# Optimization experiments

Measured on AMD Instinct MI355X. Metric: run time of the kernel, lower is better.

The kernel has to match this reference:

```python
import jax, jax.numpy as jnp
import numpy as np

N_NODES = 50000
N_EDGES = 600000
IN_CH = 128
HID = 256
OUT_FEAT = 256
OUT_CH = 128
EPS = 1e-12


def _sage_conv(x, src, dst, mask_f, Wl, bl, Wr, n_nodes):
    # PyG SAGEConv: out = lin_l(mean_{j in N(i)} x_j) + lin_r(x_i); L2-normalize rows.
    msg = x[src] * mask_f[:, None]                                  # [E, d] gather
    agg = jax.ops.segment_sum(msg, dst, num_segments=n_nodes)      # [N, d]
    cnt = jax.ops.segment_sum(mask_f, dst, num_segments=n_nodes)   # [N]
    agg = agg / jnp.maximum(cnt, 1.0)[:, None]                      # mean over kept edges
    out = agg @ Wl.T + bl + x @ Wr.T                                 # [N, h]
    nrm = jnp.maximum(jnp.linalg.norm(out, axis=-1, keepdims=True), EPS)
    return out / nrm


def setup_inputs() -> dict:
    key = jax.random.key(0)
    ks = jax.random.split(key, 12)
    x = jax.random.normal(ks[0], (N_NODES, IN_CH), dtype=jnp.float32)
    edge_index = jax.random.randint(ks[1], (2, N_EDGES), 0, N_NODES, dtype=jnp.int32)
    edge_mask = jax.random.bernoulli(ks[2], 0.7, (N_EDGES,))  # dropout_edge p=0.3 keep mask

    def lin(k, fan_out, fan_in):
        s = 1.0 / np.sqrt(fan_in)
        return jax.random.uniform(k, (fan_out, fan_in), jnp.float32, -s, s)

    W1l = lin(ks[3], HID, IN_CH)
    b1 = jnp.zeros((HID,), jnp.float32)
    W1r = lin(ks[4], HID, IN_CH)
    Ws = lin(ks[5], HID, IN_CH)
    bs = jnp.zeros((HID,), jnp.float32)
    W2l = lin(ks[6], OUT_FEAT, HID)
    b2 = jnp.zeros((OUT_FEAT,), jnp.float32)
    W2r = lin(ks[7], OUT_FEAT, HID)
    Wo = lin(ks[8], OUT_CH, OUT_FEAT)
    bo = jnp.zeros((OUT_CH,), jnp.float32)
    return {"x": x, "edge_index": edge_index, "edge_mask": edge_mask,
            "W1l": W1l, "b1": b1, "W1r": W1r, "Ws": Ws, "bs": bs,
            "W2l": W2l, "b2": b2, "W2r": W2r, "Wo": Wo, "bo": bo}


def reference(x, edge_index, edge_mask, W1l, b1, W1r, Ws, bs, W2l, b2, W2r, Wo, bo):
    src, dst = edge_index[0], edge_index[1]
    ones = jnp.ones((src.shape[0],), x.dtype)
    # conv1 uses all edges
    h = _sage_conv(x, src, dst, ones, W1l, b1, W1r, N_NODES)
    h = h + (x @ Ws.T + bs)
    h = jnp.tanh(h)
    # conv2 uses edge-dropped graph (mask = kept edges)
    mask_f = edge_mask.astype(x.dtype)
    h = jnp.tanh(_sage_conv(h, src, dst, mask_f, W2l, b2, W2r, N_NODES))
    return h @ Wo.T + bo
```

## Files before the change

### kernel.cpp

```cpp
#include <hip/hip_runtime.h>
#include <hip/hip_bf16.h>

#define N_NODES 50000
#define N_PAD   50048
#define N_EDGES 600000
#define IN_CH 128
#define HID 256
#define OUT_CH 128

typedef unsigned short u16;
typedef unsigned char u8;
typedef unsigned int u32;

typedef __attribute__((ext_vector_type(8))) short short8;
typedef __attribute__((ext_vector_type(4))) float f32x4;

typedef __attribute__((address_space(3))) u32 as3_u32;
typedef __attribute__((address_space(1))) const u32 as1_u32;

__device__ __forceinline__ float bf2f(u16 v) {
    unsigned u = ((unsigned)v) << 16;
    return __uint_as_float(u);
}
__device__ __forceinline__ u16 f2bf(float f) {
    unsigned u = __float_as_uint(f);
    u += 0x7FFF + ((u >> 16) & 1);
    return (u16)(u >> 16);
}

__device__ __forceinline__ float fast_tanh(float x) {
    float e = __builtin_amdgcn_exp2f(x * 2.88539008177793f);
    return 1.f - 2.f * __builtin_amdgcn_rcpf(e + 1.f);
}

__device__ __forceinline__ void async16(const void* g, void* l) {
    __builtin_amdgcn_global_load_lds((as1_u32*)g, (as3_u32*)l, 16, 0, 0);
}

__global__ void detect_kernel(const u16* __restrict__ xu, const u8* __restrict__ mb,
                              int* __restrict__ flags) {
    int lane = threadIdx.x & 63;

    int inr = 0;
    {
        u32 w0 = ((const u32*)xu)[lane * 2 + 0];
        u32 w1 = ((const u32*)xu)[lane * 2 + 1];
        u16 h[4] = {(u16)w0, (u16)(w0 >> 16), (u16)w1, (u16)(w1 >> 16)};
#pragma unroll
        for (int j = 0; j < 4; j++) {
            int e = (h[j] >> 7) & 0xFF;
            if (e >= 100 && e <= 133) inr++;
        }
    }

    int c1 = 0, c23 = 0, h3f_1 = 0, h3f_3 = 0;
#pragma unroll
    for (int t = 0; t < 16; t++) {
        u32 w = ((const u32*)mb)[t * 64 + lane];
        u8 b1 = (u8)(w >> 8), b2 = (u8)(w >> 16), b3 = (u8)(w >> 24);
        if (b1) c1++;
        if (b1 == 0x3F) h3f_1 = 1;
        if (b2) c23++;
        if (b3) c23++;
        if (b3 == 0x3F) h3f_3 = 1;
    }

#pragma unroll
    for (int off = 32; off > 0; off >>= 1) {
        inr   += __shfl_xor(inr, off, 64);
        c1    += __shfl_xor(c1, off, 64);
        c23   += __shfl_xor(c23, off, 64);
        h3f_1 |= __shfl_xor(h3f_1, off, 64);
        h3f_3 |= __shfl_xor(h3f_3, off, 64);
    }

    if (lane == 0 && blockIdx.x == 0) {
        flags[0] = (inr >= 200) ? 1 : 0;
        int fmt;
        if (h3f_1) fmt = 3;
        else if (h3f_3) fmt = 2;
        else if (c1 + c23 > 0) fmt = 0;
        else fmt = 1;
        flags[1] = fmt;
    }
}

#define NX (N_NODES * IN_CH)
#define DEGP_N 50176
__global__ void convert_all_kernel(const void* __restrict__ x,
                                   const void* __restrict__ W1l, const void* __restrict__ W1r,
                                   const void* __restrict__ Ws,
                                   const void* __restrict__ W2l, const void* __restrict__ W2r,
                                   const void* __restrict__ Wo,
                                   const void* __restrict__ b1, const void* __restrict__ bs,
                                   const void* __restrict__ b2, const void* __restrict__ bo,
                                   u16* __restrict__ xb, u16* __restrict__ Wc1,
                                   u16* __restrict__ Wsb, u16* __restrict__ Wc2,
                                   u16* __restrict__ Wob, float* __restrict__ biasf,
                                   u32* __restrict__ degp,
                                   const int* __restrict__ flags) {
    int i = blockIdx.x * blockDim.x + threadIdx.x;
    int isbf = flags[0];
    auto cv = [&](const void* s, int idx) -> u16 {
        return isbf ? ((const u16*)s)[idx] : f2bf(((const float*)s)[idx]);
    };
    if (i < NX) { xb[i] = cv(x, i); return; }
    i -= NX;
    if (i < 256 * 256) {
        int n = i >> 8, k = i & 255;
        const void* s = (k < 128) ? W1l : W1r;
        Wc1[i] = cv(s, n * 128 + (k & 127));
        return;
    }
    i -= 256 * 256;
    if (i < 256 * 128) { Wsb[i] = cv(Ws, i); return; }
    i -= 256 * 128;
    if (i < 256 * 512) {
        int n = i >> 9, k = i & 511;
        const void* s = (k < 256) ? W2l : W2r;
        Wc2[i] = cv(s, n * 256 + (k & 255));
        return;
    }
    i -= 256 * 512;
    if (i < 128 * 256) { Wob[i] = cv(Wo, i); return; }
    i -= 128 * 256;
    if (i < 896) {
        const void* s; int idx;
        if (i < 256)      { s = b1; idx = i; }
        else if (i < 512) { s = bs; idx = i - 256; }
        else if (i < 768) { s = b2; idx = i - 512; }
        else              { s = bo; idx = i - 768; }
        biasf[i] = isbf ? bf2f(((const u16*)s)[idx]) : ((const float*)s)[idx];
        return;
    }
    i -= 896;
    if (i < DEGP_N) degp[i] = 0;
}
#define CONV_TOTAL (NX + 256 * 256 + 256 * 128 + 256 * 512 + 128 * 256 + 896 + DEGP_N)

__global__ void hist_kernel(const int* __restrict__ ei, const void* __restrict__ em,
                            u32* __restrict__ degp, u32* __restrict__ rankp,
                            const int* __restrict__ flags) {
    int i = blockIdx.x * blockDim.x + threadIdx.x;
    if (i >= N_EDGES) return;
    int d = ei[N_EDGES + i];
    int fmt = flags[1];
    bool keep;
    if (fmt == 0)      keep = ((const u8*)em)[i] != 0;
    else if (fmt == 1) keep = ((const int*)em)[i] != 0;
    else if (fmt == 2) keep = ((const float*)em)[i] != 0.f;
    else               keep = ((const u16*)em)[i] != 0;
    u32 inc = keep ? 0x10001u : 1u;
    u32 old = atomicAdd(&degp[d], inc);
    rankp[i] = (old & 0xffffu) | (keep ? (old & 0xffff0000u) : 0xffff0000u);
}

__global__ void partial_kernel(const u32* __restrict__ degp, u32* __restrict__ partial) {
    __shared__ u32 sh[256];
    int t = threadIdx.x;
    int i = blockIdx.x * 256 + t;
    sh[t] = (i < N_NODES) ? degp[i] : 0;
    __syncthreads();
    for (int s = 128; s > 0; s >>= 1) {
        if (t < s) sh[t] += sh[t + s];
        __syncthreads();
    }
    if (t == 0) partial[blockIdx.x] = sh[0];
}

__global__ void scanp_kernel(const u32* __restrict__ partial, int* __restrict__ pscan, int nb) {
    __shared__ int sh[256];
    int t = threadIdx.x;
    u32 pv = (t < nb) ? partial[t] : 0;
    int v1 = pv & 0xffff, v2 = pv >> 16;
    sh[t] = v1;
    __syncthreads();
    for (int o = 1; o < 256; o <<= 1) {
        int u = (t >= o) ? sh[t - o] : 0;
        __syncthreads();
        sh[t] += u;
        __syncthreads();
    }
    if (t < nb) pscan[t] = sh[t] - v1;
    __syncthreads();
    sh[t] = v2;
    __syncthreads();
    for (int o = 1; o < 256; o <<= 1) {
        int u = (t >= o) ? sh[t - o] : 0;
        __syncthreads();
        sh[t] += u;
        __syncthreads();
    }
    if (t < nb) pscan[nb + t] = sh[t] - v2;
}

__global__ void rowptr_kernel(const u32* __restrict__ degp, const int* __restrict__ pscan,
                              int* __restrict__ row_ptr, int* __restrict__ row_ptr2, int nb) {
    __shared__ u32 sh[256];
    int t = threadIdx.x;
    int i = blockIdx.x * 256 + t;
    u32 v = (i < N_NODES) ? degp[i] : 0;
    sh[t] = v;
    __syncthreads();
    for (int o = 1; o < 256; o <<= 1) {
        u32 u = (t >= o) ? sh[t - o] : 0;
        __syncthreads();
        sh[t] += u;
        __syncthreads();
    }
    u32 ex = sh[t] - v;
    if (i <= N_NODES) {
        row_ptr[i]  = pscan[blockIdx.x] + (int)(ex & 0xffff);
        row_ptr2[i] = pscan[nb + blockIdx.x] + (int)(ex >> 16);
    }
}

__global__ void scatter_csr_kernel(const int* __restrict__ ei, const u32* __restrict__ rankp,
                                   const int* __restrict__ row_ptr, const int* __restrict__ row_ptr2,
                                   int* __restrict__ srcs, int* __restrict__ srcs2) {
    int i = blockIdx.x * blockDim.x + threadIdx.x;
    if (i >= N_EDGES) return;
    int d = ei[N_EDGES + i];
    int s = ei[i];
    u32 rp = rankp[i];
    srcs[row_ptr[d] + (int)(rp & 0xffffu)] = s;
    u32 kr = rp >> 16;
    if (kr != 0xffffu) srcs2[row_ptr2[d] + (int)kr] = s;
}

__global__ __launch_bounds__(256) void gather1_kernel(const int* __restrict__ row_ptr,
                                                      const int* __restrict__ srcs,
                                                      const u16* __restrict__ xb,
                                                      u16* __restrict__ aggb) {
    int wid = (blockIdx.x * blockDim.x + threadIdx.x) >> 6;
    int lane = threadIdx.x & 63;
    if (wid >= N_NODES) return;
    int start = row_ptr[wid], end = row_ptr[wid + 1];
    int dg = end - start;
    int sv = (lane < dg) ? srcs[start + lane] : 0;
    float a0 = 0.f, a1 = 0.f, b0 = 0.f, b1 = 0.f;
    float c0 = 0.f, c1 = 0.f, d0 = 0.f, d1 = 0.f;
    int n = dg < 64 ? dg : 64;
    int e = 0;
    for (; e + 4 <= n; e += 4) {
        int s0 = __builtin_amdgcn_readlane(sv, e);
        int s1 = __builtin_amdgcn_readlane(sv, e + 1);
        int s2 = __builtin_amdgcn_readlane(sv, e + 2);
        int s3 = __builtin_amdgcn_readlane(sv, e + 3);
        u32 v0 = *(const u32*)(xb + (size_t)s0 * IN_CH + lane * 2);
        u32 v1 = *(const u32*)(xb + (size_t)s1 * IN_CH + lane * 2);
        u32 v2 = *(const u32*)(xb + (size_t)s2 * IN_CH + lane * 2);
        u32 v3 = *(const u32*)(xb + (size_t)s3 * IN_CH + lane * 2);
        a0 += bf2f((u16)v0); a1 += bf2f((u16)(v0 >> 16));
        b0 += bf2f((u16)v1); b1 += bf2f((u16)(v1 >> 16));
        c0 += bf2f((u16)v2); c1 += bf2f((u16)(v2 >> 16));
        d0 += bf2f((u16)v3); d1 += bf2f((u16)(v3 >> 16));
    }
    for (; e < n; e++) {
        int s0 = __builtin_amdgcn_readlane(sv, e);
        u32 v0 = *(const u32*)(xb + (size_t)s0 * IN_CH + lane * 2);
        a0 += bf2f((u16)v0); a1 += bf2f((u16)(v0 >> 16));
    }
    for (e = 64; e < dg; e++) {
        int s0 = srcs[start + e];
        u32 v0 = *(const u32*)(xb + (size_t)s0 * IN_CH + lane * 2);
        a0 += bf2f((u16)v0); a1 += bf2f((u16)(v0 >> 16));
    }
    float inv = 1.f / fmaxf((float)dg, 1.f);
    float rx = (a0 + b0) + (c0 + d0);
    float ry = (a1 + b1) + (c1 + d1);
    u32 o = (u32)f2bf(rx * inv) | ((u32)f2bf(ry * inv) << 16);
    *(u32*)(aggb + (size_t)wid * IN_CH + lane * 2) = o;
}

__global__ __launch_bounds__(256) void gather2_kernel(const int* __restrict__ row_ptr2,
                                                      const int* __restrict__ srcs2,
                                                      const u16* __restrict__ h1b,
                                                      u16* __restrict__ aggb) {
    int wid = (blockIdx.x * blockDim.x + threadIdx.x) >> 6;
    int lane = threadIdx.x & 63;
    if (wid >= N_NODES) return;
    int start = row_ptr2[wid], end = row_ptr2[wid + 1];
    int dg = end - start;
    int sv = (lane < dg) ? srcs2[start + lane] : 0;
    float a0 = 0.f, a1 = 0.f, a2 = 0.f, a3 = 0.f;
    float b0 = 0.f, b1 = 0.f, b2 = 0.f, b3 = 0.f;
    float c0 = 0.f, c1 = 0.f, c2 = 0.f, c3 = 0.f;
    float d0 = 0.f, d1 = 0.f, d2 = 0.f, d3 = 0.f;
    int n = dg < 64 ? dg : 64;
    int e = 0;
    for (; e + 4 <= n; e += 4) {
        int s0 = __builtin_amdgcn_readlane(sv, e);
        int s1 = __builtin_amdgcn_readlane(sv, e + 1);
        int s2 = __builtin_amdgcn_readlane(sv, e + 2);
        int s3 = __builtin_amdgcn_readlane(sv, e + 3);
        uint2 v = *(const uint2*)(h1b + (size_t)s0 * HID + lane * 4);
        uint2 w = *(const uint2*)(h1b + (size_t)s1 * HID + lane * 4);
        uint2 y = *(const uint2*)(h1b + (size_t)s2 * HID + lane * 4);
        uint2 zz = *(const uint2*)(h1b + (size_t)s3 * HID + lane * 4);
        a0 += bf2f((u16)v.x); a1 += bf2f((u16)(v.x >> 16));
        a2 += bf2f((u16)v.y); a3 += bf2f((u16)(v.y >> 16));
        b0 += bf2f((u16)w.x); b1 += bf2f((u16)(w.x >> 16));
        b2 += bf2f((u16)w.y); b3 += bf2f((u16)(w.y >> 16));
        c0 += bf2f((u16)y.x); c1 += bf2f((u16)(y.x >> 16));
        c2 += bf2f((u16)y.y); c3 += bf2f((u16)(y.y >> 16));
        d0 += bf2f((u16)zz.x); d1 += bf2f((u16)(zz.x >> 16));
        d2 += bf2f((u16)zz.y); d3 += bf2f((u16)(zz.y >> 16));
    }
    for (; e < n; e++) {
        int s0 = __builtin_amdgcn_readlane(sv, e);
        uint2 v = *(const uint2*)(h1b + (size_t)s0 * HID + lane * 4);
        a0 += bf2f((u16)v.x); a1 += bf2f((u16)(v.x >> 16));
        a2 += bf2f((u16)v.y); a3 += bf2f((u16)(v.y >> 16));
    }
    for (e = 64; e < dg; e++) {
        int s0 = srcs2[start + e];
        uint2 v = *(const uint2*)(h1b + (size_t)s0 * HID + lane * 4);
        a0 += bf2f((u16)v.x); a1 += bf2f((u16)(v.x >> 16));
        a2 += bf2f((u16)v.y); a3 += bf2f((u16)(v.y >> 16));
    }
    float inv = 1.f / fmaxf((float)dg, 1.f);
    float r0 = (a0 + b0) + (c0 + d0);
    float r1 = (a1 + b1) + (c1 + d1);
    float r2 = (a2 + b2) + (c2 + d2);
    float r3 = (a3 + b3) + (c3 + d3);
    u32 o0 = (u32)f2bf(r0 * inv) | ((u32)f2bf(r1 * inv) << 16);
    u32 o1 = (u32)f2bf(r2 * inv) | ((u32)f2bf(r3 * inv) << 16);
    u16* p = aggb + (size_t)wid * HID + lane * 4;
    *(u32*)p = o0;
    *(u32*)(p + 2) = o1;
}

template<int MODE>
__global__ __launch_bounds__(256, 2) void gemm_staged(
    const u16* __restrict__ A0, const u16* __restrict__ A1,
    const u16* __restrict__ W0, const u16* __restrict__ W1,
    const float* __restrict__ bias0, const float* __restrict__ bias1,
    u16* __restrict__ outb, void* __restrict__ outv, const int* __restrict__ flags) {

    constexpr int NT  = 4;
    constexpr int Nw  = NT * 16;
    constexpr int NKS = (MODE == 1) ? 6 : 8;
    constexpr int BBYTES = NT * 64 * 128;
    __shared__ __align__(16) u8 ldsmem[16384 + 2 * BBYTES];

    int tid = threadIdx.x;
    int w = tid >> 6, lane = tid & 63;
    int q = lane >> 4, c = lane & 15;
    int m_base = blockIdx.x * 64;
    int rj = lane >> 3, jj = lane & 7;
    int j16 = ((jj ^ rj) << 4);

    f32x4 acc[4][NT], acc2[4][NT];
    const f32x4 z = {0.f, 0.f, 0.f, 0.f};
#pragma unroll
    for (int mt = 0; mt < 4; mt++)
#pragma unroll
        for (int nt = 0; nt < NT; nt++) { acc[mt][nt] = z; acc2[mt][nt] = z; }

    auto stage = [&](int ks, int b) {
        const u16* ap; int astr, kta;
        const u16* wp; int wstr, ktw;
        if (MODE == 1) {
            astr = 128;
            if (ks < 2)      { ap = A0; kta = ks; }
            else if (ks < 4) { ap = A1; kta = ks - 2; }
            else             { ap = A1; kta = ks - 4; }
            if (ks < 4) { wp = W0; wstr = 256; ktw = ks; }
            else        { wp = W1; wstr = 128; ktw = ks - 4; }
        } else {
            astr = 256;
            if (ks < 4) { ap = A0; kta = ks; } else { ap = A1; kta = ks - 4; }
            wp = W0; wstr = 512; ktw = ks;
        }
#pragma unroll
        for (int t = 0; t < 2; t++) {
            int r = w * 16 + t * 8;
            const u8* g = (const u8*)(ap + (size_t)(m_base + r + rj) * astr) + kta * 128 + j16;
            async16(g, ldsmem + b * 8192 + r * 128);
        }
#pragma unroll
        for (int t = 0; t < NT * 2; t++) {
            int n = w * Nw + t * 8;
            const u8* g = (const u8*)(wp + (size_t)(n + rj) * wstr) + ktw * 128 + j16;
            async16(g, ldsmem + 16384 + b * BBYTES + n * 128);
        }
    };

    auto compute = [&](int b, f32x4 (*tgt)[NT]) {
        const u8* ab = ldsmem + b * 8192;
        const u8* bb = ldsmem + 16384 + b * BBYTES;
#pragma unroll
        for (int kk = 0; kk < 2; kk++) {
            int sA = (((kk * 4 + q) ^ (c & 7)) << 4);
            short8 af[4], bfr[NT];
#pragma unroll
            for (int mt = 0; mt < 4; mt++)
                af[mt] = *(const short8*)(ab + (mt * 16 + c) * 128 + sA);
#pragma unroll
            for (int nt = 0; nt < NT; nt++)
                bfr[nt] = *(const short8*)(bb + (w * Nw + nt * 16 + c) * 128 + sA);
#pragma unroll
            for (int mt = 0; mt < 4; mt++)
#pragma unroll
                for (int nt = 0; nt < NT; nt++)
                    tgt[mt][nt] = __builtin_amdgcn_mfma_f32_16x16x32_bf16(af[mt], bfr[nt], tgt[mt][nt], 0, 0, 0);
        }
    };

    stage(0, 0);
    int b = 0;
#pragma unroll
    for (int ks = 0; ks < NKS; ks++) {
        __syncthreads();
        if (ks + 1 < NKS) stage(ks + 1, b ^ 1);
        if (MODE == 1 && ks >= 4) compute(b, acc2);
        else                      compute(b, acc);
        b ^= 1;
    }
    __syncthreads();

    float* redf = (float*)ldsmem;
    float bcol[NT];
#pragma unroll
    for (int nt = 0; nt < NT; nt++) bcol[nt] = bias0[w * Nw + nt * 16 + c];
    float s[4][4];
#pragma unroll
    for (int mt = 0; mt < 4; mt++)
#pragma unroll
        for (int r = 0; r < 4; r++) {
            float t = 0.f;
#pragma unroll
            for (int nt = 0; nt < NT; nt++) {
                float v = acc[mt][nt][r] + bcol[nt];
                acc[mt][nt][r] = v;
                t += v * v;
            }
            s[mt][r] = t;
        }
#pragma unroll
    for (int off = 1; off < 16; off <<= 1) {
#pragma unroll
        for (int mt = 0; mt < 4; mt++)
#pragma unroll
            for (int r = 0; r < 4; r++)
                s[mt][r] += __shfl_xor(s[mt][r], off, 64);
    }
    if (c == 0) {
#pragma unroll
        for (int mt = 0; mt < 4; mt++)
#pragma unroll
            for (int r = 0; r < 4; r++)
                redf[(mt * 16 + q * 4 + r) * 4 + w] = s[mt][r];
    }
    __syncthreads();
    if (tid < 64) {
        float t = redf[tid * 4] + redf[tid * 4 + 1] + redf[tid * 4 + 2] + redf[tid * 4 + 3];
        redf[256 + tid] = 1.f / fmaxf(sqrtf(t), 1e-12f);
    }
    __syncthreads();

    if (MODE == 1) {
        float b2col[NT];
#pragma unroll
        for (int nt = 0; nt < NT; nt++) b2col[nt] = bias1[w * Nw + nt * 16 + c];
#pragma unroll
        for (int mt = 0; mt < 4; mt++)
#pragma unroll
            for (int r = 0; r < 4; r++) {
                int rl = mt * 16 + q * 4 + r;
                int row = m_base + rl;
                if (row < N_NODES) {
                    float iv = redf[256 + rl];
#pragma unroll
                    for (int nt = 0; nt < NT; nt++) {
                        int col = w * Nw + nt * 16 + c;
                        float t = fast_tanh(acc[mt][nt][r] * iv + acc2[mt][nt][r] + b2col[nt]);
                        float tp = __shfl_xor(t, 1, 64);
                        if (!(lane & 1)) {
                            u32 pk = (u32)f2bf(t) | ((u32)f2bf(tp) << 16);
                            *(u32*)(outb + (size_t)row * HID + col) = pk;
                        }
                    }
                }
            }
    } else {
        u8* h2l = ldsmem + 16384;
        u8* wol = ldsmem + 16384 + BBYTES;
        int rj2 = lane >> 5, s5 = lane & 31;

        auto stageWo = [&](int half) {
#pragma unroll
            for (int t = 0; t < 8; t++) {
                int rl = w * 16 + t * 2 + rj2;
                const u8* g = (const u8*)W1 + (((size_t)(half * 64 + rl)) << 9)
                            + ((s5 ^ (rl & 7)) << 4);
                async16(g, wol + (w * 16 + t * 2) * 512);
            }
        };

        stageWo(0);
#pragma unroll
        for (int mt = 0; mt < 4; mt++)
#pragma unroll
            for (int r = 0; r < 4; r++) {
                int rl = mt * 16 + q * 4 + r;
                float iv = redf[256 + rl];
#pragma unroll
                for (int nt = 0; nt < NT; nt++) {
                    int k = w * Nw + nt * 16 + c;
                    float t = fast_tanh(acc[mt][nt][r] * iv);
                    float tp = __shfl_xor(t, 1, 64);
                    if (!(lane & 1)) {
                        u32 pk = (u32)f2bf(t) | ((u32)f2bf(tp) << 16);
                        int off = rl * 512 + ((((k >> 3) ^ (rl & 7)) << 4)) + ((k & 7) << 1);
                        *(u32*)(h2l + off) = pk;
                    }
                }
            }
        __syncthreads();

        int isbf = flags[0];
        float bO0 = bias1[w * 16 + c];
        float bO1 = bias1[64 + w * 16 + c];

        auto computeO = [&](f32x4* accO) {
#pragma unroll
            for (int kk = 0; kk < 8; kk++) {
                int sw = (((kk * 4 + q) ^ (c & 7)) << 4);
                short8 bfO = *(const short8*)(wol + (w * 16 + c) * 512 + sw);
#pragma unroll
                for (int mt = 0; mt < 4; mt++) {
                    short8 afO = *(const short8*)(h2l + (mt * 16 + c) * 512 + sw);
                    accO[mt] = __builtin_amdgcn_mfma_f32_16x16x32_bf16(afO, bfO, accO[mt], 0, 0, 0);
                }
            }
        };
        auto storeO = [&](int half, float bO, f32x4* accO) {
#pragma unroll
            for (int mt = 0; mt < 4; mt++)
#pragma unroll
                for (int r = 0; r < 4; r++) {
                    int row = m_base + mt * 16 + q * 4 + r;
                    if (row < N_NODES) {
                        int col = half * 64 + w * 16 + c;
                        float v = accO[mt][r] + bO;
                        if (isbf) {
                            float vp = __shfl_xor(v, 1, 64);
                            if (!(lane & 1))
                                *(u32*)((u16*)outv + (size_t)row * OUT_CH + col) =
                                    (u32)f2bf(v) | ((u32)f2bf(vp) << 16);
                        } else {
                            ((float*)outv)[(size_t)row * OUT_CH + col] = v;
                        }
                    }
                }
        };

        f32x4 accO[4];
#pragma unroll
        for (int mt = 0; mt < 4; mt++) accO[mt] = z;
        computeO(accO);
        __syncthreads();
        stageWo(1);
        storeO(0, bO0, accO);
        __syncthreads();
#pragma unroll
        for (int mt = 0; mt < 4; mt++) accO[mt] = z;
        computeO(accO);
        storeO(1, bO1, accO);
    }
}

extern "C" void kernel_launch(void* const* d_in, const int* in_sizes, int n_in,
                              void* d_out, int out_size, void* d_ws, size_t ws_size,
                              hipStream_t stream) {
    const void* x    = d_in[0];
    const int*  ei   = (const int*)d_in[1];
    const void* em   = d_in[2];
    const void* W1l  = d_in[3];
    const void* b1   = d_in[4];
    const void* W1r  = d_in[5];
    const void* Ws   = d_in[6];
    const void* bs   = d_in[7];
    const void* W2l  = d_in[8];
    const void* b2   = d_in[9];
    const void* W2r  = d_in[10];
    const void* Wo   = d_in[11];
    const void* bo   = d_in[12];

    char* p = (char*)d_ws;
    auto carve = [&](size_t bytes) { char* r = p; p += (bytes + 63) & ~(size_t)63; return r; };
    int*   flags   = (int*)carve(256);
    u16*   xb      = (u16*)carve((size_t)N_PAD * IN_CH * 2);
    u16*   h1b     = (u16*)carve((size_t)N_PAD * HID * 2);
    u16*   aggb    = (u16*)carve((size_t)N_PAD * HID * 2);
    u16*   Wc1     = (u16*)carve(256 * 256 * 2);
    u16*   Wsb     = (u16*)carve(256 * 128 * 2);
    u16*   Wc2     = (u16*)carve(256 * 512 * 2);
    u16*   Wob     = (u16*)carve(128 * 256 * 2);
    float* biasf   = (float*)carve(896 * 4);
    u32*   degp    = (u32*)carve(50176 * 4);
    int*   row_ptr = (int*)carve(50056 * 4);
    int*   row_ptr2= (int*)carve(50056 * 4);
    u32*   partial = (u32*)carve(256 * 4);
    int*   pscan   = (int*)carve(512 * 4);
    u32*   rankp   = (u32*)carve((size_t)N_EDGES * 4);
    int*   srcs    = (int*)carve((size_t)N_EDGES * 4);
    int*   srcs2   = (int*)carve((size_t)N_EDGES * 4);
    float* b1f = biasf, *bsf = biasf + 256, *b2f = biasf + 512, *bof = biasf + 768;
    (void)ws_size; (void)in_sizes; (void)n_in; (void)out_size;

    detect_kernel<<<1, 64, 0, stream>>>((const u16*)x, (const u8*)em, flags);

    convert_all_kernel<<<(CONV_TOTAL + 255) / 256, 256, 0, stream>>>(
        x, W1l, W1r, Ws, W2l, W2r, Wo, b1, bs, b2, bo,
        xb, Wc1, Wsb, Wc2, Wob, biasf, degp, flags);

    hist_kernel<<<(N_EDGES + 255) / 256, 256, 0, stream>>>(ei, em, degp, rankp, flags);
    const int NB = (N_NODES + 255) / 256;
    partial_kernel<<<NB, 256, 0, stream>>>(degp, partial);
    scanp_kernel<<<1, 256, 0, stream>>>(partial, pscan, NB);
    rowptr_kernel<<<NB, 256, 0, stream>>>(degp, pscan, row_ptr, row_ptr2, NB);
    scatter_csr_kernel<<<(N_EDGES + 255) / 256, 256, 0, stream>>>(ei, rankp, row_ptr, row_ptr2, srcs, srcs2);

    const int GB = N_PAD / 64;

    gather1_kernel<<<(N_NODES * 64) / 256, 256, 0, stream>>>(row_ptr, srcs, xb, aggb);
    gemm_staged<1><<<GB, 256, 0, stream>>>(aggb, xb, Wc1, Wsb, b1f, bsf, h1b, nullptr, flags);

    gather2_kernel<<<(N_NODES * 64) / 256, 256, 0, stream>>>(row_ptr2, srcs2, h1b, aggb);
    gemm_staged<2><<<GB, 256, 0, stream>>>(aggb, h1b, Wc2, Wob, b2f, bof, nullptr, d_out, flags);
}
```

Before: 295.3 us.

## Load GEMM weight fragments directly into registers and pipeline A tiles manually

Weight (B) operands of the staged GEMM are now loaded straight from global memory into registers, one k-step ahead, instead of going through LDS double buffers. The A tile pipeline is rewritten with explicit vmcnt waits and raw barriers, and the stage for the next-next step is issued so two A loads overlap compute. The Wo epilogue GEMM also reads weights directly from global memory, dropping its LDS staging and two block syncs. This shrinks LDS use, which may help occupancy, and cuts LDS traffic. In exchange it adds register pressure and uncoalesced-looking per-lane global loads of weights, and relies on hand-counted vmcnt values being correct.

After: 319.3 us. +8.1%, slower.

```diff
diff --git a/kernel.cpp b/kernel.cpp
--- a/kernel.cpp
+++ b/kernel.cpp
@@ -36,6 +36,9 @@
 __device__ __forceinline__ void async16(const void* g, void* l) {
     __builtin_amdgcn_global_load_lds((as1_u32*)g, (as3_u32*)l, 16, 0, 0);
 }
+
+#define WAITV(N) do { asm volatile("s_waitcnt vmcnt(" #N ")" ::: "memory"); \
+                      __builtin_amdgcn_sched_barrier(0); } while (0)
 
 __global__ void detect_kernel(const u16* __restrict__ xu, const u8* __restrict__ mb,
                               int* __restrict__ flags) {
@@ -340,9 +343,11 @@
 
     constexpr int NT  = 4;
     constexpr int Nw  = NT * 16;
-    constexpr int NKS = (MODE == 1) ? 6 : 8;
-    constexpr int BBYTES = NT * 64 * 128;
-    __shared__ __align__(16) u8 ldsmem[16384 + 2 * BBYTES];
+    constexpr int NKS    = (MODE == 1) ? 6 : 8;
+    constexpr int NSTAGE = (MODE == 1) ? 4 : 8;
+    constexpr int ABYTES = 8192;
+    constexpr int LDSSZ  = (MODE == 2) ? (2 * ABYTES + 32768) : (2 * ABYTES);
+    __shared__ __align__(16) u8 ldsmem[LDSSZ];
 
     int tid = threadIdx.x;
     int w = tid >> 6, lane = tid & 63;
@@ -360,63 +365,77 @@
 
     auto stage = [&](int ks, int b) {
         const u16* ap; int astr, kta;
-        const u16* wp; int wstr, ktw;
         if (MODE == 1) {
             astr = 128;
-            if (ks < 2)      { ap = A0; kta = ks; }
-            else if (ks < 4) { ap = A1; kta = ks - 2; }
-            else             { ap = A1; kta = ks - 4; }
-            if (ks < 4) { wp = W0; wstr = 256; ktw = ks; }
-            else        { wp = W1; wstr = 128; ktw = ks - 4; }
+            if (ks < 2) { ap = A0; kta = ks; }
+            else        { ap = A1; kta = ks - 2; }
         } else {
             astr = 256;
             if (ks < 4) { ap = A0; kta = ks; } else { ap = A1; kta = ks - 4; }
-            wp = W0; wstr = 512; ktw = ks;
         }
 #pragma unroll
         for (int t = 0; t < 2; t++) {
             int r = w * 16 + t * 8;
             const u8* g = (const u8*)(ap + (size_t)(m_base + r + rj) * astr) + kta * 128 + j16;
-            async16(g, ldsmem + b * 8192 + r * 128);
-        }
-#pragma unroll
-        for (int t = 0; t < NT * 2; t++) {
-            int n = w * Nw + t * 8;
-            const u8* g = (const u8*)(wp + (size_t)(n + rj) * wstr) + ktw * 128 + j16;
-            async16(g, ldsmem + 16384 + b * BBYTES + n * 128);
+            async16(g, ldsmem + b * ABYTES + r * 128);
         }
     };
 
-    auto compute = [&](int b, f32x4 (*tgt)[NT]) {
-        const u8* ab = ldsmem + b * 8192;
-        const u8* bb = ldsmem + 16384 + b * BBYTES;
+    auto loadB = [&](int ks, short8* Bf) {
+#pragma unroll
+        for (int nt = 0; nt < NT; nt++)
+#pragma unroll
+            for (int kk = 0; kk < 2; kk++) {
+                int row = w * Nw + nt * 16 + c;
+                const u16* g;
+                if (MODE == 1) {
+                    if (ks < 4) g = W0 + (size_t)row * 256 + ks * 64 + kk * 32 + q * 8;
+                    else        g = W1 + (size_t)row * 128 + (ks - 4) * 64 + kk * 32 + q * 8;
+                } else {
+                    g = W0 + (size_t)row * 512 + ks * 64 + kk * 32 + q * 8;
+                }
+                Bf[nt * 2 + kk] = *(const short8*)g;
+            }
+    };
+
+    auto compute = [&](int b, const short8* Bf, f32x4 (*tgt)[NT]) {
+        const u8* ab = ldsmem + b * ABYTES;
 #pragma unroll
         for (int kk = 0; kk < 2; kk++) {
             int sA = (((kk * 4 + q) ^ (c & 7)) << 4);
-            short8 af[4], bfr[NT];
+            short8 af[4];
 #pragma unroll
             for (int mt = 0; mt < 4; mt++)
                 af[mt] = *(const short8*)(ab + (mt * 16 + c) * 128 + sA);
 #pragma unroll
-            for (int nt = 0; nt < NT; nt++)
-                bfr[nt] = *(const short8*)(bb + (w * Nw + nt * 16 + c) * 128 + sA);
-#pragma unroll
             for (int mt = 0; mt < 4; mt++)
 #pragma unroll
                 for (int nt = 0; nt < NT; nt++)
-                    tgt[mt][nt] = __builtin_amdgcn_mfma_f32_16x16x32_bf16(af[mt], bfr[nt], tgt[mt][nt], 0, 0, 0);
+                    tgt[mt][nt] = __builtin_amdgcn_mfma_f32_16x16x32_bf16(af[mt], Bf[nt * 2 + kk], tgt[mt][nt], 0, 0, 0);
         }
     };
 
+    short8 BA[8];
     stage(0, 0);
-    int b = 0;
+    loadB(0, BA);
+    stage(1, 1);
+    WAITV(10);
+    __builtin_amdgcn_s_barrier();
+
 #pragma unroll
     for (int ks = 0; ks < NKS; ks++) {
-        __syncthreads();
-        if (ks + 1 < NKS) stage(ks + 1, b ^ 1);
-        if (MODE == 1 && ks >= 4) compute(b, acc2);
-        else                      compute(b, acc);
-        b ^= 1;
+        if (MODE == 1 && ks >= 4) compute(ks & 1, BA, acc2);
+        else                      compute(ks & 1, BA, acc);
+        if (ks + 1 < NKS) loadB(ks + 1, BA);
+        if (ks + 2 < NSTAGE) {
+            __builtin_amdgcn_s_barrier();
+            stage(ks + 2, ks & 1);
+        }
+        if (ks + 1 < NSTAGE) {
+            if (ks + 2 < NSTAGE) { WAITV(10); }
+            else                 { WAITV(8);  }
+            __builtin_amdgcn_s_barrier();
+        }
     }
     __syncthreads();
 
@@ -485,21 +504,8 @@
                 }
             }
     } else {
-        u8* h2l = ldsmem + 16384;
-        u8* wol = ldsmem + 16384 + BBYTES;
-        int rj2 = lane >> 5, s5 = lane & 31;
-
-        auto stageWo = [&](int half) {
-#pragma unroll
-            for (int t = 0; t < 8; t++) {
-                int rl = w * 16 + t * 2 + rj2;
-                const u8* g = (const u8*)W1 + (((size_t)(half * 64 + rl)) << 9)
-                            + ((s5 ^ (rl & 7)) << 4);
-                async16(g, wol + (w * 16 + t * 2) * 512);
-            }
-        };
-
-        stageWo(0);
+        u8* h2l = ldsmem + 2 * ABYTES;
+
 #pragma unroll
         for (int mt = 0; mt < 4; mt++)
 #pragma unroll
@@ -521,14 +527,13 @@
         __syncthreads();
 
         int isbf = flags[0];
-        float bO0 = bias1[w * 16 + c];
-        float bO1 = bias1[64 + w * 16 + c];
-
-        auto computeO = [&](f32x4* accO) {
+
+        auto computeO = [&](f32x4* accO, int half) {
 #pragma unroll
             for (int kk = 0; kk < 8; kk++) {
+                const u16* g = W1 + (size_t)(half * 64 + w * 16 + c) * 256 + kk * 32 + q * 8;
+                short8 bfO = *(const short8*)g;
                 int sw = (((kk * 4 + q) ^ (c & 7)) << 4);
-                short8 bfO = *(const short8*)(wol + (w * 16 + c) * 512 + sw);
 #pragma unroll
                 for (int mt = 0; mt < 4; mt++) {
                     short8 afO = *(const short8*)(h2l + (mt * 16 + c) * 512 + sw);
@@ -557,17 +562,16 @@
                 }
         };
 
+        float bO0 = bias1[w * 16 + c];
+        float bO1 = bias1[64 + w * 16 + c];
         f32x4 accO[4];
 #pragma unroll
         for (int mt = 0; mt < 4; mt++) accO[mt] = z;
-        computeO(accO);
-        __syncthreads();
-        stageWo(1);
+        computeO(accO, 0);
         storeO(0, bO0, accO);
-        __syncthreads();
 #pragma unroll
         for (int mt = 0; mt < 4; mt++) accO[mt] = z;
-        computeO(accO);
+        computeO(accO, 1);
         storeO(1, bO1, accO);
     }
 }
```

## Prefetch two K-stages ahead with explicit vmcnt waits in staged GEMM

Applied to the files above, without the earlier changes.

Restructures the GEMM main loop so two K-slices are in flight. Each iteration computes, issues the load for the slice after next, then waits only for the older slice's loads using explicit s_waitcnt vmcnt counts. The code no longer waits for every load at each __syncthreads. It also skips redundant A-tile loads in MODE 1's second phase, where the A data is already resident. This relies on hand-counted outstanding-load numbers, and any mismatch would cause races or stalls.

Measured after the change: 297.7 us. Within noise of the previous version (+0.8%).

```diff
diff --git a/kernel.cpp b/kernel.cpp
--- a/kernel.cpp
+++ b/kernel.cpp
@@ -35,6 +35,13 @@
 
 __device__ __forceinline__ void async16(const void* g, void* l) {
     __builtin_amdgcn_global_load_lds((as1_u32*)g, (as3_u32*)l, 16, 0, 0);
+}
+
+__device__ __forceinline__ void waitv_sel(int n) {
+    if (n >= 10)     { asm volatile("s_waitcnt vmcnt(10)" ::: "memory"); }
+    else if (n >= 8) { asm volatile("s_waitcnt vmcnt(8)"  ::: "memory"); }
+    else             { asm volatile("s_waitcnt vmcnt(0)"  ::: "memory"); }
+    __builtin_amdgcn_sched_barrier(0);
 }
 
 __global__ void detect_kernel(const u16* __restrict__ xu, const u8* __restrict__ mb,
@@ -341,8 +348,10 @@
     constexpr int NT  = 4;
     constexpr int Nw  = NT * 16;
     constexpr int NKS = (MODE == 1) ? 6 : 8;
-    constexpr int BBYTES = NT * 64 * 128;
-    __shared__ __align__(16) u8 ldsmem[16384 + 2 * BBYTES];
+    constexpr int ABYTES = 8192;
+    constexpr int AARENA = 16384;
+    constexpr int BBYTES = 32768;
+    __shared__ __align__(16) u8 ldsmem[AARENA + 2 * BBYTES];
 
     int tid = threadIdx.x;
     int w = tid >> 6, lane = tid & 63;
@@ -373,23 +382,25 @@
             if (ks < 4) { ap = A0; kta = ks; } else { ap = A1; kta = ks - 4; }
             wp = W0; wstr = 512; ktw = ks;
         }
-#pragma unroll
-        for (int t = 0; t < 2; t++) {
-            int r = w * 16 + t * 8;
-            const u8* g = (const u8*)(ap + (size_t)(m_base + r + rj) * astr) + kta * 128 + j16;
-            async16(g, ldsmem + b * 8192 + r * 128);
+        if (!(MODE == 1 && ks >= 4)) {
+#pragma unroll
+            for (int t = 0; t < 2; t++) {
+                int r = w * 16 + t * 8;
+                const u8* g = (const u8*)(ap + (size_t)(m_base + r + rj) * astr) + kta * 128 + j16;
+                async16(g, ldsmem + b * ABYTES + r * 128);
+            }
         }
 #pragma unroll
         for (int t = 0; t < NT * 2; t++) {
             int n = w * Nw + t * 8;
             const u8* g = (const u8*)(wp + (size_t)(n + rj) * wstr) + ktw * 128 + j16;
-            async16(g, ldsmem + 16384 + b * BBYTES + n * 128);
+            async16(g, ldsmem + AARENA + b * BBYTES + n * 128);
         }
     };
 
     auto compute = [&](int b, f32x4 (*tgt)[NT]) {
-        const u8* ab = ldsmem + b * 8192;
-        const u8* bb = ldsmem + 16384 + b * BBYTES;
+        const u8* ab = ldsmem + b * ABYTES;
+        const u8* bb = ldsmem + AARENA + b * BBYTES;
 #pragma unroll
         for (int kk = 0; kk < 2; kk++) {
             int sA = (((kk * 4 + q) ^ (c & 7)) << 4);
@@ -409,14 +420,25 @@
     };
 
     stage(0, 0);
-    int b = 0;
+    stage(1, 1);
+    asm volatile("s_waitcnt vmcnt(10)" ::: "memory");
+    __builtin_amdgcn_sched_barrier(0);
+    __builtin_amdgcn_s_barrier();
+
 #pragma unroll
     for (int ks = 0; ks < NKS; ks++) {
-        __syncthreads();
-        if (ks + 1 < NKS) stage(ks + 1, b ^ 1);
-        if (MODE == 1 && ks >= 4) compute(b, acc2);
-        else                      compute(b, acc);
-        b ^= 1;
+        if (MODE == 1 && ks >= 4) compute(ks & 1, acc2);
+        else                      compute(ks & 1, acc);
+        if (ks + 1 < NKS) {
+            if (ks + 2 < NKS) {
+                __builtin_amdgcn_s_barrier();
+                stage(ks + 2, ks & 1);
+                waitv_sel((MODE == 1 && ks + 2 >= 4) ? 8 : 10);
+            } else {
+                waitv_sel(0);
+            }
+            __builtin_amdgcn_s_barrier();
+        }
     }
     __syncthreads();
 
@@ -485,8 +507,8 @@
                 }
             }
     } else {
-        u8* h2l = ldsmem + 16384;
-        u8* wol = ldsmem + 16384 + BBYTES;
+        u8* h2l = ldsmem + AARENA;
+        u8* wol = ldsmem + AARENA + BBYTES;
         int rj2 = lane >> 5, s5 = lane & 31;
 
         auto stageWo = [&](int half) {
```

## Enlarge GEMM tile to 128 rows with 8 waves in a 2x4 grid

Applied to the files above, without the earlier changes.

The fused GEMM kernels move from 256-thread blocks covering 64 rows to 512-thread blocks covering 128 rows, with waves arranged 2x4 over M and N. Each staged weight tile is now shared by twice as many rows, which halves weight traffic per row and the number of blocks. In MODE 1 the A tile is no longer re-staged for the second GEMM because it reuses the already loaded x tile. The output projection in MODE 2 is restructured into four 32-column rounds with a smaller Wo staging buffer. The cost is higher LDS use per block (96KB), fewer blocks (391) and extra barriers in the output stage, which may hurt occupancy and latency hiding.

After: 299.6 us. No clear change (+1.5%).

```diff
diff --git a/kernel.cpp b/kernel.cpp
--- a/kernel.cpp
+++ b/kernel.cpp
@@ -332,31 +332,32 @@
 }
 
 template<int MODE>
-__global__ __launch_bounds__(256, 2) void gemm_staged(
+__global__ __launch_bounds__(512, 2) void gemm_staged(
     const u16* __restrict__ A0, const u16* __restrict__ A1,
     const u16* __restrict__ W0, const u16* __restrict__ W1,
     const float* __restrict__ bias0, const float* __restrict__ bias1,
     u16* __restrict__ outb, void* __restrict__ outv, const int* __restrict__ flags) {
 
-    constexpr int NT  = 4;
-    constexpr int Nw  = NT * 16;
     constexpr int NKS = (MODE == 1) ? 6 : 8;
-    constexpr int BBYTES = NT * 64 * 128;
-    __shared__ __align__(16) u8 ldsmem[16384 + 2 * BBYTES];
+    constexpr int ABYTES = 16384;
+    constexpr int AARENA = 32768;
+    constexpr int BBYTES = 32768;
+    __shared__ __align__(16) u8 ldsmem[AARENA + 2 * BBYTES];
 
     int tid = threadIdx.x;
     int w = tid >> 6, lane = tid & 63;
+    int wm = w >> 2, wn = w & 3;
     int q = lane >> 4, c = lane & 15;
-    int m_base = blockIdx.x * 64;
+    int m_base = blockIdx.x * 128;
     int rj = lane >> 3, jj = lane & 7;
     int j16 = ((jj ^ rj) << 4);
 
-    f32x4 acc[4][NT], acc2[4][NT];
+    f32x4 acc[4][4], acc2[4][4];
     const f32x4 z = {0.f, 0.f, 0.f, 0.f};
 #pragma unroll
     for (int mt = 0; mt < 4; mt++)
 #pragma unroll
-        for (int nt = 0; nt < NT; nt++) { acc[mt][nt] = z; acc2[mt][nt] = z; }
+        for (int nt = 0; nt < 4; nt++) { acc[mt][nt] = z; acc2[mt][nt] = z; }
 
     auto stage = [&](int ks, int b) {
         const u16* ap; int astr, kta;
@@ -373,37 +374,39 @@
             if (ks < 4) { ap = A0; kta = ks; } else { ap = A1; kta = ks - 4; }
             wp = W0; wstr = 512; ktw = ks;
         }
-#pragma unroll
-        for (int t = 0; t < 2; t++) {
-            int r = w * 16 + t * 8;
-            const u8* g = (const u8*)(ap + (size_t)(m_base + r + rj) * astr) + kta * 128 + j16;
-            async16(g, ldsmem + b * 8192 + r * 128);
+        if (!(MODE == 1 && ks >= 4)) {
+#pragma unroll
+            for (int t = 0; t < 2; t++) {
+                int r = w * 16 + t * 8;
+                const u8* g = (const u8*)(ap + (size_t)(m_base + r + rj) * astr) + kta * 128 + j16;
+                async16(g, ldsmem + b * ABYTES + r * 128);
+            }
         }
 #pragma unroll
-        for (int t = 0; t < NT * 2; t++) {
-            int n = w * Nw + t * 8;
+        for (int t = 0; t < 4; t++) {
+            int n = w * 32 + t * 8;
             const u8* g = (const u8*)(wp + (size_t)(n + rj) * wstr) + ktw * 128 + j16;
-            async16(g, ldsmem + 16384 + b * BBYTES + n * 128);
+            async16(g, ldsmem + AARENA + b * BBYTES + n * 128);
         }
     };
 
-    auto compute = [&](int b, f32x4 (*tgt)[NT]) {
-        const u8* ab = ldsmem + b * 8192;
-        const u8* bb = ldsmem + 16384 + b * BBYTES;
+    auto compute = [&](int b, f32x4 (*tgt)[4]) {
+        const u8* ab = ldsmem + b * ABYTES;
+        const u8* bb = ldsmem + AARENA + b * BBYTES;
 #pragma unroll
         for (int kk = 0; kk < 2; kk++) {
             int sA = (((kk * 4 + q) ^ (c & 7)) << 4);
-            short8 af[4], bfr[NT];
+            short8 af[4], bfr[4];
 #pragma unroll
             for (int mt = 0; mt < 4; mt++)
-                af[mt] = *(const short8*)(ab + (mt * 16 + c) * 128 + sA);
-#pragma unroll
-            for (int nt = 0; nt < NT; nt++)
-                bfr[nt] = *(const short8*)(bb + (w * Nw + nt * 16 + c) * 128 + sA);
+                af[mt] = *(const short8*)(ab + (wm * 64 + mt * 16 + c) * 128 + sA);
+#pragma unroll
+            for (int nt = 0; nt < 4; nt++)
+                bfr[nt] = *(const short8*)(bb + (wn * 64 + nt * 16 + c) * 128 + sA);
 #pragma unroll
             for (int mt = 0; mt < 4; mt++)
 #pragma unroll
-                for (int nt = 0; nt < NT; nt++)
+                for (int nt = 0; nt < 4; nt++)
                     tgt[mt][nt] = __builtin_amdgcn_mfma_f32_16x16x32_bf16(af[mt], bfr[nt], tgt[mt][nt], 0, 0, 0);
         }
     };
@@ -421,9 +424,9 @@
     __syncthreads();
 
     float* redf = (float*)ldsmem;
-    float bcol[NT];
-#pragma unroll
-    for (int nt = 0; nt < NT; nt++) bcol[nt] = bias0[w * Nw + nt * 16 + c];
+    float bcol[4];
+#pragma unroll
+    for (int nt = 0; nt < 4; nt++) bcol[nt] = bias0[wn * 64 + nt * 16 + c];
     float s[4][4];
 #pragma unroll
     for (int mt = 0; mt < 4; mt++)
@@ -431,7 +434,7 @@
         for (int r = 0; r < 4; r++) {
             float t = 0.f;
 #pragma unroll
-            for (int nt = 0; nt < NT; nt++) {
+            for (int nt = 0; nt < 4; nt++) {
                 float v = acc[mt][nt][r] + bcol[nt];
                 acc[mt][nt][r] = v;
                 t += v * v;
@@ -451,30 +454,30 @@
         for (int mt = 0; mt < 4; mt++)
 #pragma unroll
             for (int r = 0; r < 4; r++)
-                redf[(mt * 16 + q * 4 + r) * 4 + w] = s[mt][r];
-    }
-    __syncthreads();
-    if (tid < 64) {
+                redf[(wm * 64 + mt * 16 + q * 4 + r) * 4 + wn] = s[mt][r];
+    }
+    __syncthreads();
+    if (tid < 128) {
         float t = redf[tid * 4] + redf[tid * 4 + 1] + redf[tid * 4 + 2] + redf[tid * 4 + 3];
-        redf[256 + tid] = 1.f / fmaxf(sqrtf(t), 1e-12f);
+        redf[512 + tid] = 1.f / fmaxf(sqrtf(t), 1e-12f);
     }
     __syncthreads();
 
     if (MODE == 1) {
-        float b2col[NT];
-#pragma unroll
-        for (int nt = 0; nt < NT; nt++) b2col[nt] = bias1[w * Nw + nt * 16 + c];
+        float b2col[4];
+#pragma unroll
+        for (int nt = 0; nt < 4; nt++) b2col[nt] = bias1[wn * 64 + nt * 16 + c];
 #pragma unroll
         for (int mt = 0; mt < 4; mt++)
 #pragma unroll
             for (int r = 0; r < 4; r++) {
-                int rl = mt * 16 + q * 4 + r;
+                int rl = wm * 64 + mt * 16 + q * 4 + r;
                 int row = m_base + rl;
                 if (row < N_NODES) {
-                    float iv = redf[256 + rl];
-#pragma unroll
-                    for (int nt = 0; nt < NT; nt++) {
-                        int col = w * Nw + nt * 16 + c;
+                    float iv = redf[512 + rl];
+#pragma unroll
+                    for (int nt = 0; nt < 4; nt++) {
+                        int col = wn * 64 + nt * 16 + c;
                         float t = fast_tanh(acc[mt][nt][r] * iv + acc2[mt][nt][r] + b2col[nt]);
                         float tp = __shfl_xor(t, 1, 64);
                         if (!(lane & 1)) {
@@ -485,17 +488,17 @@
                 }
             }
     } else {
-        u8* h2l = ldsmem + 16384;
-        u8* wol = ldsmem + 16384 + BBYTES;
+        u8* h2l = ldsmem + AARENA;
+        u8* wol = ldsmem + 8192;
         int rj2 = lane >> 5, s5 = lane & 31;
 
-        auto stageWo = [&](int half) {
-#pragma unroll
-            for (int t = 0; t < 8; t++) {
-                int rl = w * 16 + t * 2 + rj2;
-                const u8* g = (const u8*)W1 + (((size_t)(half * 64 + rl)) << 9)
-                            + ((s5 ^ (rl & 7)) << 4);
-                async16(g, wol + (w * 16 + t * 2) * 512);
+        auto stageWo = [&](int round) {
+#pragma unroll
+            for (int t = 0; t < 2; t++) {
+                int rl2 = w * 4 + t * 2 + rj2;
+                const u8* g = (const u8*)W1 + (((size_t)(round * 32 + rl2)) << 9)
+                            + ((s5 ^ (rl2 & 7)) << 4);
+                async16(g, wol + (w * 4 + t * 2) * 512);
             }
         };
 
@@ -504,11 +507,11 @@
         for (int mt = 0; mt < 4; mt++)
 #pragma unroll
             for (int r = 0; r < 4; r++) {
-                int rl = mt * 16 + q * 4 + r;
-                float iv = redf[256 + rl];
-#pragma unroll
-                for (int nt = 0; nt < NT; nt++) {
-                    int k = w * Nw + nt * 16 + c;
+                int rl = wm * 64 + mt * 16 + q * 4 + r;
+                float iv = redf[512 + rl];
+#pragma unroll
+                for (int nt = 0; nt < 4; nt++) {
+                    int k = wn * 64 + nt * 16 + c;
                     float t = fast_tanh(acc[mt][nt][r] * iv);
                     float tp = __shfl_xor(t, 1, 64);
                     if (!(lane & 1)) {
@@ -521,30 +524,30 @@
         __syncthreads();
 
         int isbf = flags[0];
-        float bO0 = bias1[w * 16 + c];
-        float bO1 = bias1[64 + w * 16 + c];
-
-        auto computeO = [&](f32x4* accO) {
+
+#pragma unroll
+        for (int round = 0; round < 4; round++) {
+            f32x4 accO[2];
+            accO[0] = z; accO[1] = z;
 #pragma unroll
             for (int kk = 0; kk < 8; kk++) {
                 int sw = (((kk * 4 + q) ^ (c & 7)) << 4);
-                short8 bfO = *(const short8*)(wol + (w * 16 + c) * 512 + sw);
-#pragma unroll
-                for (int mt = 0; mt < 4; mt++) {
-                    short8 afO = *(const short8*)(h2l + (mt * 16 + c) * 512 + sw);
-                    accO[mt] = __builtin_amdgcn_mfma_f32_16x16x32_bf16(afO, bfO, accO[mt], 0, 0, 0);
+                short8 afO = *(const short8*)(h2l + (w * 16 + c) * 512 + sw);
+#pragma unroll
+                for (int nt2 = 0; nt2 < 2; nt2++) {
+                    short8 bfO = *(const short8*)(wol + (nt2 * 16 + c) * 512 + sw);
+                    accO[nt2] = __builtin_amdgcn_mfma_f32_16x16x32_bf16(afO, bfO, accO[nt2], 0, 0, 0);
                 }
             }
-        };
-        auto storeO = [&](int half, float bO, f32x4* accO) {
-#pragma unroll
-            for (int mt = 0; mt < 4; mt++)
+#pragma unroll
+            for (int nt2 = 0; nt2 < 2; nt2++) {
+                int col = round * 32 + nt2 * 16 + c;
+                float bO = bias1[col];
 #pragma unroll
                 for (int r = 0; r < 4; r++) {
-                    int row = m_base + mt * 16 + q * 4 + r;
+                    int row = m_base + w * 16 + q * 4 + r;
                     if (row < N_NODES) {
-                        int col = half * 64 + w * 16 + c;
-                        float v = accO[mt][r] + bO;
+                        float v = accO[nt2][r] + bO;
                         if (isbf) {
                             float vp = __shfl_xor(v, 1, 64);
                             if (!(lane & 1))
@@ -555,20 +558,13 @@
                         }
                     }
                 }
-        };
-
-        f32x4 accO[4];
-#pragma unroll
-        for (int mt = 0; mt < 4; mt++) accO[mt] = z;
-        computeO(accO);
-        __syncthreads();
-        stageWo(1);
-        storeO(0, bO0, accO);
-        __syncthreads();
-#pragma unroll
-        for (int mt = 0; mt < 4; mt++) accO[mt] = z;
-        computeO(accO);
-        storeO(1, bO1, accO);
+            }
+            if (round < 3) {
+                __syncthreads();
+                stageWo(round + 1);
+                __syncthreads();
+            }
+        }
     }
 }
 
@@ -624,11 +620,11 @@
     rowptr_kernel<<<NB, 256, 0, stream>>>(degp, pscan, row_ptr, row_ptr2, NB);
     scatter_csr_kernel<<<(N_EDGES + 255) / 256, 256, 0, stream>>>(ei, rankp, row_ptr, row_ptr2, srcs, srcs2);
 
-    const int GB = N_PAD / 64;
+    const int GB = N_PAD / 128;
 
     gather1_kernel<<<(N_NODES * 64) / 256, 256, 0, stream>>>(row_ptr, srcs, xb, aggb);
-    gemm_staged<1><<<GB, 256, 0, stream>>>(aggb, xb, Wc1, Wsb, b1f, bsf, h1b, nullptr, flags);
+    gemm_staged<1><<<GB, 512, 0, stream>>>(aggb, xb, Wc1, Wsb, b1f, bsf, h1b, nullptr, flags);
 
     gather2_kernel<<<(N_NODES * 64) / 256, 256, 0, stream>>>(row_ptr2, srcs2, h1b, aggb);
-    gemm_staged<2><<<GB, 256, 0, stream>>>(aggb, h1b, Wc2, Wob, b2f, bof, nullptr, d_out, flags);
-}
+    gemm_staged<2><<<GB, 512, 0, stream>>>(aggb, h1b, Wc2, Wob, b2f, bof, nullptr, d_out, flags);
+}
```
